# Performance work log

Measured on AMD Instinct MI355X. Metric: run time of the kernel, lower is better.

The kernel has to match this reference:

```python
import jax, jax.numpy as jnp
import numpy as np

D_MODEL = 1024
D_FF = 4096
NUM_EXPERTS = 8
TOP_K = 2
LN_EPS = 1e-5


def setup_inputs() -> dict:
    key = jax.random.key(0)
    ks = jax.random.split(key, 8)
    B, S = 4, 2048
    x = jax.random.normal(ks[0], (B, S, D_MODEL), dtype=jnp.float32)
    router_w = jax.random.normal(ks[1], (D_MODEL, NUM_EXPERTS), dtype=jnp.float32) * (1.0 / np.sqrt(D_MODEL))
    router_b = jnp.zeros((NUM_EXPERTS,), dtype=jnp.float32)
    w1 = jax.random.normal(ks[2], (NUM_EXPERTS, D_MODEL, D_FF), dtype=jnp.float32) * (1.0 / np.sqrt(D_MODEL))
    b1 = jnp.zeros((NUM_EXPERTS, D_FF), dtype=jnp.float32)
    w2 = jax.random.normal(ks[3], (NUM_EXPERTS, D_FF, D_MODEL), dtype=jnp.float32) * (1.0 / np.sqrt(D_FF))
    b2 = jnp.zeros((NUM_EXPERTS, D_MODEL), dtype=jnp.float32)
    gamma = jnp.ones((D_MODEL,), dtype=jnp.float32)
    beta = jnp.zeros((D_MODEL,), dtype=jnp.float32)
    return {"x": x, "router_w": router_w, "router_b": router_b,
            "w1": w1, "b1": b1, "w2": w2, "b2": b2,
            "gamma": gamma, "beta": beta}


def reference(x, router_w, router_b, w1, b1, w2, b2, gamma, beta):
    B, S, D = x.shape
    E = w1.shape[0]
    xf = x.reshape(B * S, D)  # [T, D]

    # Router: linear -> softmax -> top-k (scores are softmax probs of selected experts)
    logits = xf @ router_w + router_b                     # [T, E]
    probs = jax.nn.softmax(logits, axis=-1)
    scores, idx = jax.lax.top_k(probs, TOP_K)             # [T, K]

    # Dense combine weights: comb[t, e] = sum_k scores[t,k] * (idx[t,k]==e)
    comb = (jax.nn.one_hot(idx, E, dtype=x.dtype) * scores[..., None]).sum(axis=1)  # [T, E]

    # Dispatch/compute/combine. comb is 0 for unrouted (token, expert) pairs,
    # so the weighted sum matches the gather/scatter loop in the original.
    out = jnp.zeros_like(xf)
    for e in range(E):  # fixed small expert count, structurally distinct weights
        h = jax.nn.gelu(xf @ w1[e] + b1[e])               # [T, D_FF]
        out = out + comb[:, e:e + 1] * (h @ w2[e] + b2[e])
    out = out.reshape(B, S, D)

    # residual + LayerNorm (dropout = 0.0)
    y = x + out
    mu = y.mean(axis=-1, keepdims=True)
    var = ((y - mu) ** 2).mean(axis=-1, keepdims=True)
    z = (y - mu) * jax.lax.rsqrt(var + LN_EPS) * gamma + beta

    # routing decision export (bool mask over experts, jit-friendly stand-in for a Python set)
    selected = comb.sum(axis=0) > 0
    return z, selected
```

## Files before the change

### kernel.cpp

```cpp
#include <hip/hip_runtime.h>


#define T_TOKENS 8192
#define DM 1024
#define DF 4096
#define NE 8

typedef unsigned short u16;
typedef short v8s __attribute__((ext_vector_type(8)));
typedef float v4f __attribute__((ext_vector_type(4)));

__device__ __forceinline__ u16 f2bf(float f) {
  unsigned u = __float_as_uint(f);
  u += 0x7FFFu + ((u >> 16) & 1u);
  return (u16)(u >> 16);
}

__device__ __forceinline__ void load16_lds(const u16* g, u16* lds) {
  __builtin_amdgcn_global_load_lds(
      (const __attribute__((address_space(1))) unsigned int*)g,
      (__attribute__((address_space(3))) unsigned int*)lds, 16, 0, 0);
}

__global__ __launch_bounds__(256) void router_kernel(
    const float* __restrict__ x, const float* __restrict__ rw,
    const float* __restrict__ rb, int* __restrict__ counts,
    int* __restrict__ list_token, int* __restrict__ epos,
    float* __restrict__ escore, u16* __restrict__ xb) {
  int w = threadIdx.x >> 6, lane = threadIdx.x & 63;
  int t = blockIdx.x * 4 + w;
  const float* xr = x + (size_t)t * DM;
  u16* xbr = xb + (size_t)t * DM;
  float a[8] = {0.f, 0.f, 0.f, 0.f, 0.f, 0.f, 0.f, 0.f};
  for (int j = lane; j < DM; j += 64) {
    float xv = xr[j];
    xbr[j] = f2bf(xv);
    const float4* r4 = (const float4*)(rw + (size_t)j * 8);
    float4 w0 = r4[0], w1 = r4[1];
    a[0] += xv * w0.x; a[1] += xv * w0.y; a[2] += xv * w0.z; a[3] += xv * w0.w;
    a[4] += xv * w1.x; a[5] += xv * w1.y; a[6] += xv * w1.z; a[7] += xv * w1.w;
  }
#pragma unroll
  for (int e = 0; e < 8; e++)
#pragma unroll
    for (int off = 32; off > 0; off >>= 1) a[e] += __shfl_down(a[e], off);
  if (lane == 0) {
    float l[8];
    float mx = -1e30f;
#pragma unroll
    for (int e = 0; e < 8; e++) { l[e] = a[e] + rb[e]; mx = fmaxf(mx, l[e]); }
    float sum = 0.f;
#pragma unroll
    for (int e = 0; e < 8; e++) { l[e] = __expf(l[e] - mx); sum += l[e]; }
    float inv = 1.f / sum;
    int i1 = 0; float p1 = -1.f;
#pragma unroll
    for (int e = 0; e < 8; e++) if (l[e] > p1) { p1 = l[e]; i1 = e; }
    int i2 = -1; float p2 = -1.f;
#pragma unroll
    for (int e = 0; e < 8; e++) if (e != i1 && l[e] > p2) { p2 = l[e]; i2 = e; }
    int pos1 = atomicAdd(&counts[i1], 1);
    int pos2 = atomicAdd(&counts[i2], 1);
    list_token[i1 * T_TOKENS + pos1] = t;
    list_token[i2 * T_TOKENS + pos2] = t;
    epos[2 * t] = (i1 << 16) | pos1;
    epos[2 * t + 1] = (i2 << 16) | pos2;
    escore[2 * t] = p1 * inv;
    escore[2 * t + 1] = p2 * inv;
  }
}

__global__ __launch_bounds__(64) void finalize_kernel(const int* __restrict__ counts,
                                                      int* __restrict__ offsets,
                                                      float* __restrict__ sel_out) {
  int tid = threadIdx.x;
  if (tid == 0) {
    int o = 0;
    for (int e = 0; e < NE; e++) { offsets[e] = o; o += counts[e]; }
    offsets[NE] = o;
  }
  if (tid < NE) sel_out[tid] = counts[tid] > 0 ? 1.f : 0.f;
}

__global__ __launch_bounds__(256) void transpose_cvt_kernel(
    const float* __restrict__ src, u16* __restrict__ dst, int R, int C) {
  __shared__ float tile[64 * 65];
  int e = blockIdx.z;
  const float* s = src + (size_t)e * R * C;
  u16* d = dst + (size_t)e * R * C;
  int r0 = blockIdx.y * 64, c0 = blockIdx.x * 64;
  int tid = threadIdx.x;
  int pr = tid >> 4, pc4 = (tid & 15) * 4;
#pragma unroll
  for (int i = 0; i < 4; i++) {
    int r = pr + i * 16;
    float4 v = *(const float4*)(s + (size_t)(r0 + r) * C + c0 + pc4);
    tile[r * 65 + pc4] = v.x;
    tile[r * 65 + pc4 + 1] = v.y;
    tile[r * 65 + pc4 + 2] = v.z;
    tile[r * 65 + pc4 + 3] = v.w;
  }
  __syncthreads();
  int r8 = (tid & 7) * 8, cb = tid >> 3;
#pragma unroll
  for (int i = 0; i < 2; i++) {
    int c = cb + i * 32;
    unsigned pk0 = (unsigned)f2bf(tile[(r8 + 0) * 65 + c]) |
                   ((unsigned)f2bf(tile[(r8 + 1) * 65 + c]) << 16);
    unsigned pk1 = (unsigned)f2bf(tile[(r8 + 2) * 65 + c]) |
                   ((unsigned)f2bf(tile[(r8 + 3) * 65 + c]) << 16);
    unsigned pk2 = (unsigned)f2bf(tile[(r8 + 4) * 65 + c]) |
                   ((unsigned)f2bf(tile[(r8 + 5) * 65 + c]) << 16);
    unsigned pk3 = (unsigned)f2bf(tile[(r8 + 6) * 65 + c]) |
                   ((unsigned)f2bf(tile[(r8 + 7) * 65 + c]) << 16);
    *(uint4*)(d + (size_t)(c0 + c) * R + r0 + r8) = make_uint4(pk0, pk1, pk2, pk3);
  }
}

__global__ __launch_bounds__(256) void gemm1_kernel(
    const u16* __restrict__ xb, const u16* __restrict__ w1t,
    const float* __restrict__ b1, const int* __restrict__ counts,
    const int* __restrict__ offsets, const int* __restrict__ list_token,
    u16* __restrict__ H) {
  int e = blockIdx.z;
  int cnt = counts[e];
  int r0 = blockIdx.y * 128;
  if (r0 >= cnt) return;
  int n0 = blockIdx.x * 128;
  int rem = cnt - r0;

  __shared__ __align__(16) u16 As[128 * 32];
  __shared__ __align__(16) u16 Bs[128 * 32];

  int tid = threadIdx.x;
  int ra0 = tid >> 2, ca0 = tid & 3;
  int ra1 = ra0 + 64;
  const int* lst = list_token + e * T_TOKENS + r0;
  int tok0 = (ra0 < rem) ? lst[ra0] : lst[0];
  int tok1 = (ra1 < rem) ? lst[ra1] : lst[0];
  const u16* gA0 = xb + (size_t)tok0 * DM + ca0 * 8;
  const u16* gA1 = xb + (size_t)tok1 * DM + ca0 * 8;
  const u16* gB0 = w1t + ((size_t)e * DF + n0 + ra0) * DM + ca0 * 8;
  const u16* gB1 = w1t + ((size_t)e * DF + n0 + ra1) * DM + ca0 * 8;

  int lane = tid & 63, wv = tid >> 6;
  u16* ldsA0 = As + wv * 512;
  u16* ldsA1 = As + 2048 + wv * 512;
  u16* ldsB0 = Bs + wv * 512;
  u16* ldsB1 = Bs + 2048 + wv * 512;

  int wm = (wv >> 1) * 64, wn = (wv & 1) * 64;
  int ml = lane & 15, quad = lane >> 4;

  v4f acc[4][4];
#pragma unroll
  for (int i = 0; i < 4; i++)
#pragma unroll
    for (int j = 0; j < 4; j++) acc[i][j] = (v4f){0.f, 0.f, 0.f, 0.f};

  for (int k0 = 0; k0 < DM; k0 += 32) {
    load16_lds(gA0 + k0, ldsA0);
    load16_lds(gA1 + k0, ldsA1);
    load16_lds(gB0 + k0, ldsB0);
    load16_lds(gB1 + k0, ldsB1);
    __syncthreads();
    v8s af[4], bf[4];
#pragma unroll
    for (int i = 0; i < 4; i++)
      af[i] = *(const v8s*)&As[(wm + i * 16 + ml) * 32 + quad * 8];
#pragma unroll
    for (int j = 0; j < 4; j++)
      bf[j] = *(const v8s*)&Bs[(wn + j * 16 + ml) * 32 + quad * 8];
#pragma unroll
    for (int i = 0; i < 4; i++)
#pragma unroll
      for (int j = 0; j < 4; j++)
        acc[i][j] = __builtin_amdgcn_mfma_f32_16x16x32_bf16(af[i], bf[j], acc[i][j], 0, 0, 0);
    __syncthreads();
  }

  int slotbase = offsets[e] + r0;
#pragma unroll
  for (int i = 0; i < 4; i++) {
    int rbase = wm + i * 16 + quad * 4;
#pragma unroll
    for (int j = 0; j < 4; j++) {
      int cc = n0 + wn + j * 16 + ml;
      float bias = b1[e * DF + cc];
#pragma unroll
      for (int r = 0; r < 4; r++) {
        int row = rbase + r;
        float v = acc[i][j][r] + bias;
        float u = 0.7978845608028654f * (v + 0.044715f * v * v * v);
        float h = v / (1.f + __expf(-2.f * u));
        float hp = __shfl_xor(h, 1);
        if (((ml & 1) == 0) && row < rem) {
          unsigned pk = (unsigned)f2bf(h) | ((unsigned)f2bf(hp) << 16);
          *(unsigned*)&H[(size_t)(slotbase + row) * DF + cc] = pk;
        }
      }
    }
  }
}

__global__ __launch_bounds__(256) void gemm2_kernel(
    const u16* __restrict__ H, const u16* __restrict__ w2t,
    const float* __restrict__ b2, const int* __restrict__ counts,
    const int* __restrict__ offsets, float* __restrict__ partial) {
  int e = blockIdx.z;
  int cnt = counts[e];
  int r0 = blockIdx.y * 128;
  if (r0 >= cnt) return;
  int n0 = blockIdx.x * 128;
  int rem = cnt - r0;
  int slotbase = offsets[e] + r0;

  __shared__ __align__(16) u16 As[128 * 32];
  __shared__ __align__(16) u16 Bs[128 * 32];

  int tid = threadIdx.x;
  int ra0 = tid >> 2, ca0 = tid & 3;
  int ra1 = ra0 + 64;
  int ar0 = (ra0 < rem) ? ra0 : 0;
  int ar1 = (ra1 < rem) ? ra1 : 0;
  const u16* gA0 = H + (size_t)(slotbase + ar0) * DF + ca0 * 8;
  const u16* gA1 = H + (size_t)(slotbase + ar1) * DF + ca0 * 8;
  const u16* gB0 = w2t + ((size_t)e * DM + n0 + ra0) * DF + ca0 * 8;
  const u16* gB1 = w2t + ((size_t)e * DM + n0 + ra1) * DF + ca0 * 8;

  int lane = tid & 63, wv = tid >> 6;
  u16* ldsA0 = As + wv * 512;
  u16* ldsA1 = As + 2048 + wv * 512;
  u16* ldsB0 = Bs + wv * 512;
  u16* ldsB1 = Bs + 2048 + wv * 512;

  int wm = (wv >> 1) * 64, wn = (wv & 1) * 64;
  int ml = lane & 15, quad = lane >> 4;

  v4f acc[4][4];
#pragma unroll
  for (int i = 0; i < 4; i++)
#pragma unroll
    for (int j = 0; j < 4; j++) acc[i][j] = (v4f){0.f, 0.f, 0.f, 0.f};

  for (int k0 = 0; k0 < DF; k0 += 32) {
    load16_lds(gA0 + k0, ldsA0);
    load16_lds(gA1 + k0, ldsA1);
    load16_lds(gB0 + k0, ldsB0);
    load16_lds(gB1 + k0, ldsB1);
    __syncthreads();
    v8s af[4], bf[4];
#pragma unroll
    for (int i = 0; i < 4; i++)
      af[i] = *(const v8s*)&As[(wm + i * 16 + ml) * 32 + quad * 8];
#pragma unroll
    for (int j = 0; j < 4; j++)
      bf[j] = *(const v8s*)&Bs[(wn + j * 16 + ml) * 32 + quad * 8];
#pragma unroll
    for (int i = 0; i < 4; i++)
#pragma unroll
      for (int j = 0; j < 4; j++)
        acc[i][j] = __builtin_amdgcn_mfma_f32_16x16x32_bf16(af[i], bf[j], acc[i][j], 0, 0, 0);
    __syncthreads();
  }

#pragma unroll
  for (int i = 0; i < 4; i++) {
    int rbase = wm + i * 16 + quad * 4;
#pragma unroll
    for (int j = 0; j < 4; j++) {
      int cc = n0 + wn + j * 16 + ml;
      float bias = b2[e * DM + cc];
#pragma unroll
      for (int r = 0; r < 4; r++) {
        int row = rbase + r;
        if (row < rem)
          partial[(size_t)(slotbase + row) * DM + cc] = acc[i][j][r] + bias;
      }
    }
  }
}

__global__ __launch_bounds__(256) void ln_kernel(
    const float* __restrict__ x, const float* __restrict__ partial,
    const int* __restrict__ offsets, const int* __restrict__ epos,
    const float* __restrict__ escore, const float* __restrict__ gamma,
    const float* __restrict__ beta, float* __restrict__ out) {
  int t = blockIdx.x;
  int tid = threadIdx.x;
  int e0p = epos[2 * t], e1p = epos[2 * t + 1];
  float s0 = escore[2 * t], s1 = escore[2 * t + 1];
  size_t row0 = (size_t)offsets[e0p >> 16] + (e0p & 0xFFFF);
  size_t row1 = (size_t)offsets[e1p >> 16] + (e1p & 0xFFFF);
  float4 xv = ((const float4*)(x + (size_t)t * DM))[tid];
  float4 p0 = ((const float4*)(partial + row0 * DM))[tid];
  float4 p1 = ((const float4*)(partial + row1 * DM))[tid];
  float4 y;
  y.x = xv.x + s0 * p0.x + s1 * p1.x;
  y.y = xv.y + s0 * p0.y + s1 * p1.y;
  y.z = xv.z + s0 * p0.z + s1 * p1.z;
  y.w = xv.w + s0 * p0.w + s1 * p1.w;
  float s = y.x + y.y + y.z + y.w;
  float ss = y.x * y.x + y.y * y.y + y.z * y.z + y.w * y.w;
#pragma unroll
  for (int off = 32; off > 0; off >>= 1) {
    s += __shfl_down(s, off);
    ss += __shfl_down(ss, off);
  }
  __shared__ float red[10];
  int wid = tid >> 6, lane = tid & 63;
  if (lane == 0) { red[wid] = s; red[4 + wid] = ss; }
  __syncthreads();
  if (tid == 0) {
    float S = red[0] + red[1] + red[2] + red[3];
    float SS = red[4] + red[5] + red[6] + red[7];
    float mu = S * (1.f / DM);
    float var = SS * (1.f / DM) - mu * mu;
    red[8] = mu;
    red[9] = rsqrtf(var + 1e-5f);
  }
  __syncthreads();
  float mu = red[8], rs = red[9];
  float4 g = ((const float4*)gamma)[tid];
  float4 b = ((const float4*)beta)[tid];
  float4 z;
  z.x = (y.x - mu) * rs * g.x + b.x;
  z.y = (y.y - mu) * rs * g.y + b.y;
  z.z = (y.z - mu) * rs * g.z + b.z;
  z.w = (y.w - mu) * rs * g.w + b.w;
  ((float4*)(out + (size_t)t * DM))[tid] = z;
}

extern "C" void kernel_launch(void* const* d_in, const int* in_sizes, int n_in,
                              void* d_out, int out_size, void* d_ws, size_t ws_size,
                              hipStream_t stream) {
  const float* x = (const float*)d_in[0];
  const float* rw = (const float*)d_in[1];
  const float* rb = (const float*)d_in[2];
  const float* w1 = (const float*)d_in[3];
  const float* b1 = (const float*)d_in[4];
  const float* w2 = (const float*)d_in[5];
  const float* b2 = (const float*)d_in[6];
  const float* gamma = (const float*)d_in[7];
  const float* beta = (const float*)d_in[8];
  float* out = (float*)d_out;

  char* ws = (char*)d_ws;
  int* counts = (int*)(ws + 0);
  int* offsets = (int*)(ws + 256);
  int* list_token = (int*)(ws + 4096);
  int* epos = (int*)(ws + 266240);
  float* escore = (float*)(ws + 331776);
  u16* xb = (u16*)(ws + 1048576);
  u16* w1t = (u16*)(ws + 17825792);
  u16* w2t = (u16*)(ws + 84934656);
  u16* H = (u16*)(ws + 152043520);
  float* partial = (float*)(ws + 286261248);

  hipMemsetAsync(counts, 0, NE * sizeof(int), stream);

  router_kernel<<<dim3(T_TOKENS / 4), dim3(256), 0, stream>>>(
      x, rw, rb, counts, list_token, epos, escore, xb);
  finalize_kernel<<<dim3(1), dim3(64), 0, stream>>>(
      counts, offsets, out + (size_t)T_TOKENS * DM);
  transpose_cvt_kernel<<<dim3(64, 16, NE), dim3(256), 0, stream>>>(w1, w1t, DM, DF);
  transpose_cvt_kernel<<<dim3(16, 64, NE), dim3(256), 0, stream>>>(w2, w2t, DF, DM);

  gemm1_kernel<<<dim3(DF / 128, 64, NE), dim3(256), 0, stream>>>(
      xb, w1t, b1, counts, offsets, list_token, H);
  gemm2_kernel<<<dim3(DM / 128, 64, NE), dim3(256), 0, stream>>>(
      H, w2t, b2, counts, offsets, partial);
  ln_kernel<<<dim3(T_TOKENS), dim3(256), 0, stream>>>(x, partial, offsets, epos,
                                                      escore, gamma, beta, out);
}
```

Measured before the change: 1.010 ms.

## Widen GEMM K-tile to 64 with XOR-swizzled LDS layout

Both expert GEMM kernels now stage a 64-wide K slice per iteration instead of 32. This halves the number of barrier pairs per K loop. The global-to-LDS load mapping is reorganised so each wave loads 32 rows, and 16-byte chunks are XOR-swizzled by row so the MFMA fragment reads avoid LDS bank conflicts. The GEMM1 epilogue drops the shuffle-and-pack store and writes single bf16 values instead, which may cost store efficiency. LDS use per block doubles, which can limit occupancy.

```diff
diff --git a/kernel.cpp b/kernel.cpp
--- a/kernel.cpp
+++ b/kernel.cpp
@@ -129,28 +129,30 @@
   int n0 = blockIdx.x * 128;
   int rem = cnt - r0;
 
-  __shared__ __align__(16) u16 As[128 * 32];
-  __shared__ __align__(16) u16 Bs[128 * 32];
-
-  int tid = threadIdx.x;
-  int ra0 = tid >> 2, ca0 = tid & 3;
-  int ra1 = ra0 + 64;
+  __shared__ __align__(16) u16 As[128 * 64];
+  __shared__ __align__(16) u16 Bs[128 * 64];
+
+  int tid = threadIdx.x;
+  int lane = tid & 63, wv = tid >> 6;
+  int l3 = lane >> 3;
+  int chunk = (lane & 7) ^ l3;
+
   const int* lst = list_token + e * T_TOKENS + r0;
-  int tok0 = (ra0 < rem) ? lst[ra0] : lst[0];
-  int tok1 = (ra1 < rem) ? lst[ra1] : lst[0];
-  const u16* gA0 = xb + (size_t)tok0 * DM + ca0 * 8;
-  const u16* gA1 = xb + (size_t)tok1 * DM + ca0 * 8;
-  const u16* gB0 = w1t + ((size_t)e * DF + n0 + ra0) * DM + ca0 * 8;
-  const u16* gB1 = w1t + ((size_t)e * DF + n0 + ra1) * DM + ca0 * 8;
-
-  int lane = tid & 63, wv = tid >> 6;
-  u16* ldsA0 = As + wv * 512;
-  u16* ldsA1 = As + 2048 + wv * 512;
-  u16* ldsB0 = Bs + wv * 512;
-  u16* ldsB1 = Bs + 2048 + wv * 512;
+  const u16* gA[4];
+  const u16* gB[4];
+#pragma unroll
+  for (int j = 0; j < 4; j++) {
+    int r = wv * 32 + j * 8 + l3;
+    int tok = (r < rem) ? lst[r] : lst[0];
+    gA[j] = xb + (size_t)tok * DM + chunk * 8;
+    gB[j] = w1t + ((size_t)e * DF + n0 + r) * DM + chunk * 8;
+  }
+  u16* ldsA = As + wv * 2048;
+  u16* ldsB = Bs + wv * 2048;
 
   int wm = (wv >> 1) * 64, wn = (wv & 1) * 64;
   int ml = lane & 15, quad = lane >> 4;
+  int px = ml & 7;
 
   v4f acc[4][4];
 #pragma unroll
@@ -158,24 +160,28 @@
 #pragma unroll
     for (int j = 0; j < 4; j++) acc[i][j] = (v4f){0.f, 0.f, 0.f, 0.f};
 
-  for (int k0 = 0; k0 < DM; k0 += 32) {
-    load16_lds(gA0 + k0, ldsA0);
-    load16_lds(gA1 + k0, ldsA1);
-    load16_lds(gB0 + k0, ldsB0);
-    load16_lds(gB1 + k0, ldsB1);
+  for (int k0 = 0; k0 < DM; k0 += 64) {
+#pragma unroll
+    for (int j = 0; j < 4; j++) {
+      load16_lds(gA[j] + k0, ldsA + j * 512);
+      load16_lds(gB[j] + k0, ldsB + j * 512);
+    }
     __syncthreads();
-    v8s af[4], bf[4];
-#pragma unroll
-    for (int i = 0; i < 4; i++)
-      af[i] = *(const v8s*)&As[(wm + i * 16 + ml) * 32 + quad * 8];
-#pragma unroll
-    for (int j = 0; j < 4; j++)
-      bf[j] = *(const v8s*)&Bs[(wn + j * 16 + ml) * 32 + quad * 8];
-#pragma unroll
-    for (int i = 0; i < 4; i++)
+#pragma unroll
+    for (int s = 0; s < 2; s++) {
+      v8s af[4], bf[4];
+#pragma unroll
+      for (int i = 0; i < 4; i++)
+        af[i] = *(const v8s*)&As[(wm + i * 16 + ml) * 64 + ((s * 4 + quad) ^ px) * 8];
 #pragma unroll
       for (int j = 0; j < 4; j++)
-        acc[i][j] = __builtin_amdgcn_mfma_f32_16x16x32_bf16(af[i], bf[j], acc[i][j], 0, 0, 0);
+        bf[j] = *(const v8s*)&Bs[(wn + j * 16 + ml) * 64 + ((s * 4 + quad) ^ px) * 8];
+#pragma unroll
+      for (int i = 0; i < 4; i++)
+#pragma unroll
+        for (int j = 0; j < 4; j++)
+          acc[i][j] = __builtin_amdgcn_mfma_f32_16x16x32_bf16(af[i], bf[j], acc[i][j], 0, 0, 0);
+    }
     __syncthreads();
   }
 
@@ -190,13 +196,11 @@
 #pragma unroll
       for (int r = 0; r < 4; r++) {
         int row = rbase + r;
-        float v = acc[i][j][r] + bias;
-        float u = 0.7978845608028654f * (v + 0.044715f * v * v * v);
-        float h = v / (1.f + __expf(-2.f * u));
-        float hp = __shfl_xor(h, 1);
-        if (((ml & 1) == 0) && row < rem) {
-          unsigned pk = (unsigned)f2bf(h) | ((unsigned)f2bf(hp) << 16);
-          *(unsigned*)&H[(size_t)(slotbase + row) * DF + cc] = pk;
+        if (row < rem) {
+          float v = acc[i][j][r] + bias;
+          float u = 0.7978845608028654f * (v + 0.044715f * v * v * v);
+          float h = v / (1.f + __expf(-2.f * u));
+          H[(size_t)(slotbase + row) * DF + cc] = f2bf(h);
         }
       }
     }
@@ -215,27 +219,29 @@
   int rem = cnt - r0;
   int slotbase = offsets[e] + r0;
 
-  __shared__ __align__(16) u16 As[128 * 32];
-  __shared__ __align__(16) u16 Bs[128 * 32];
-
-  int tid = threadIdx.x;
-  int ra0 = tid >> 2, ca0 = tid & 3;
-  int ra1 = ra0 + 64;
-  int ar0 = (ra0 < rem) ? ra0 : 0;
-  int ar1 = (ra1 < rem) ? ra1 : 0;
-  const u16* gA0 = H + (size_t)(slotbase + ar0) * DF + ca0 * 8;
-  const u16* gA1 = H + (size_t)(slotbase + ar1) * DF + ca0 * 8;
-  const u16* gB0 = w2t + ((size_t)e * DM + n0 + ra0) * DF + ca0 * 8;
-  const u16* gB1 = w2t + ((size_t)e * DM + n0 + ra1) * DF + ca0 * 8;
-
+  __shared__ __align__(16) u16 As[128 * 64];
+  __shared__ __align__(16) u16 Bs[128 * 64];
+
+  int tid = threadIdx.x;
   int lane = tid & 63, wv = tid >> 6;
-  u16* ldsA0 = As + wv * 512;
-  u16* ldsA1 = As + 2048 + wv * 512;
-  u16* ldsB0 = Bs + wv * 512;
-  u16* ldsB1 = Bs + 2048 + wv * 512;
+  int l3 = lane >> 3;
+  int chunk = (lane & 7) ^ l3;
+
+  const u16* gA[4];
+  const u16* gB[4];
+#pragma unroll
+  for (int j = 0; j < 4; j++) {
+    int r = wv * 32 + j * 8 + l3;
+    int ar = (r < rem) ? r : 0;
+    gA[j] = H + (size_t)(slotbase + ar) * DF + chunk * 8;
+    gB[j] = w2t + ((size_t)e * DM + n0 + r) * DF + chunk * 8;
+  }
+  u16* ldsA = As + wv * 2048;
+  u16* ldsB = Bs + wv * 2048;
 
   int wm = (wv >> 1) * 64, wn = (wv & 1) * 64;
   int ml = lane & 15, quad = lane >> 4;
+  int px = ml & 7;
 
   v4f acc[4][4];
 #pragma unroll
@@ -243,24 +249,28 @@
 #pragma unroll
     for (int j = 0; j < 4; j++) acc[i][j] = (v4f){0.f, 0.f, 0.f, 0.f};
 
-  for (int k0 = 0; k0 < DF; k0 += 32) {
-    load16_lds(gA0 + k0, ldsA0);
-    load16_lds(gA1 + k0, ldsA1);
-    load16_lds(gB0 + k0, ldsB0);
-    load16_lds(gB1 + k0, ldsB1);
+  for (int k0 = 0; k0 < DF; k0 += 64) {
+#pragma unroll
+    for (int j = 0; j < 4; j++) {
+      load16_lds(gA[j] + k0, ldsA + j * 512);
+      load16_lds(gB[j] + k0, ldsB + j * 512);
+    }
     __syncthreads();
-    v8s af[4], bf[4];
-#pragma unroll
-    for (int i = 0; i < 4; i++)
-      af[i] = *(const v8s*)&As[(wm + i * 16 + ml) * 32 + quad * 8];
-#pragma unroll
-    for (int j = 0; j < 4; j++)
-      bf[j] = *(const v8s*)&Bs[(wn + j * 16 + ml) * 32 + quad * 8];
-#pragma unroll
-    for (int i = 0; i < 4; i++)
+#pragma unroll
+    for (int s = 0; s < 2; s++) {
+      v8s af[4], bf[4];
+#pragma unroll
+      for (int i = 0; i < 4; i++)
+        af[i] = *(const v8s*)&As[(wm + i * 16 + ml) * 64 + ((s * 4 + quad) ^ px) * 8];
 #pragma unroll
       for (int j = 0; j < 4; j++)
-        acc[i][j] = __builtin_amdgcn_mfma_f32_16x16x32_bf16(af[i], bf[j], acc[i][j], 0, 0, 0);
+        bf[j] = *(const v8s*)&Bs[(wn + j * 16 + ml) * 64 + ((s * 4 + quad) ^ px) * 8];
+#pragma unroll
+      for (int i = 0; i < 4; i++)
+#pragma unroll
+        for (int j = 0; j < 4; j++)
+          acc[i][j] = __builtin_amdgcn_mfma_f32_16x16x32_bf16(af[i], bf[j], acc[i][j], 0, 0, 0);
+    }
     __syncthreads();
   }
 
```

Measured after the change: 1.095 ms. +8.4%, slower.
